# Kernel tuning notes

Hardware: AMD Instinct MI355X
Metric: run time of the kernel (lower is better)

The kernel has to match this reference:

```python
import jax, jax.numpy as jnp
import numpy as np


def setup_inputs() -> dict:
    key = jax.random.key(0)
    ks = jax.random.split(key, 7)
    B, T, D, H = 32, 512, 512, 512
    return {
        "x": jax.random.normal(ks[0], (B, T, D), dtype=jnp.float32),
        "W_Du": jax.random.normal(ks[1], (D, H), dtype=jnp.float32) * (1.0 / np.sqrt(D)),
        "W_Dr1": jax.random.normal(ks[2], (D, H), dtype=jnp.float32) * (1.0 / np.sqrt(D)),
        "W_Dr2": jax.random.normal(ks[3], (D, H), dtype=jnp.float32) * (1.0 / np.sqrt(D)),
        "b_Du": jax.random.normal(ks[4], (H,), dtype=jnp.float32) * 0.02,
        "b_Dr1": jax.random.normal(ks[5], (H,), dtype=jnp.float32) * 0.02,
        "b_Dr2": jax.random.normal(ks[6], (H,), dtype=jnp.float32) * 0.02,
    }


def reference(x, W_Du, W_Dr1, W_Dr2, b_Du, b_Dr1, b_Dr2):
    # Precompute all per-step projections across time (batched matmuls),
    # then run the strictly sequential gated recurrence with lax.scan.
    r1 = jax.nn.softmax(jnp.einsum('btd,dh->bth', x, W_Dr1) + b_Dr1, axis=-1)  # [B,T,H]
    r2 = jax.nn.softmax(jnp.einsum('btd,dh->bth', x, W_Dr2) + b_Dr2, axis=-1)  # [B,T,H]
    u = jnp.tanh(jnp.einsum('btd,dh->bth', x, W_Du) + b_Du)                     # [B,T,H]

    def step(s, inp):
        r1t, r2t, ut = inp
        s_new = r1t * s + r2t * ut
        return s_new, s_new

    init = jnp.zeros((x.shape[0], W_Du.shape[1]), dtype=x.dtype)
    # time-major for scan: [T,B,H]
    _, ys = jax.lax.scan(
        step, init,
        (jnp.swapaxes(r1, 0, 1), jnp.swapaxes(r2, 0, 1), jnp.swapaxes(u, 0, 1)),
    )
    return jnp.swapaxes(ys, 0, 1)  # [B,T,H]
```

## Files before the change

kernel.cpp:

```cpp
#include <hip/hip_runtime.h>
#include <hip/hip_bf16.h>

#define B_N 32
#define T_N 512
#define D_N 512
#define H_N 512
#define M_N (B_N * T_N)

typedef __attribute__((ext_vector_type(8))) short bf16x8;
typedef __attribute__((ext_vector_type(4))) float f32x4;

__device__ __forceinline__ unsigned short f2bf(float f) {
  unsigned u = __float_as_uint(f);
  u += 0x7FFFu + ((u >> 16) & 1u);
  return (unsigned short)(u >> 16);
}
__device__ __forceinline__ float bf2f(unsigned short h) {
  return __uint_as_float(((unsigned)h) << 16);
}
__device__ __forceinline__ unsigned short f2h(float f) {
  _Float16 h = (_Float16)f;
  return *(unsigned short*)&h;
}
__device__ __forceinline__ float h2f(unsigned short u) {
  _Float16 h = *(_Float16*)&u;
  return (float)h;
}

#define GLOAD16(g, l) __builtin_amdgcn_global_load_lds( \
    (const __attribute__((address_space(1))) void*)(g), \
    (__attribute__((address_space(3))) void*)(l), 16, 0, 0)

__global__ void prep_kernel(const float* __restrict__ x,
                            const float* __restrict__ W0,
                            const float* __restrict__ W1,
                            const float* __restrict__ W2,
                            unsigned short* __restrict__ xb,
                            unsigned short* __restrict__ Wt) {
  int blk = blockIdx.x;
  int tid = threadIdx.x;
  if (blk < 768) {
    __shared__ float tile[32][33];
    int id = blk >> 8;
    int t = blk & 255;
    int kr = (t >> 4) << 5;
    int nc = (t & 15) << 5;
    const float* W = (id == 0) ? W0 : (id == 1) ? W1 : W2;
    unsigned short* Wo = Wt + (size_t)id * (D_N * H_N);
    int tx = tid & 31, ty0 = tid >> 5;
    for (int ty = ty0; ty < 32; ty += 8)
      tile[ty][tx] = W[(size_t)(kr + ty) * H_N + nc + tx];
    __syncthreads();
    for (int ty = ty0; ty < 32; ty += 8)
      Wo[(size_t)(nc + ty) * D_N + kr + tx] = f2bf(tile[tx][ty]);
  } else {
    int b = blk - 768;
    const float4* xv = (const float4*)x;
#pragma unroll
    for (int u = 0; u < 4; ++u) {
      int i = b * 1024 + u * 256 + tid;
      float4 v = xv[i];
      ushort4 o;
      o.x = f2bf(v.x); o.y = f2bf(v.y); o.z = f2bf(v.z); o.w = f2bf(v.w);
      ((ushort4*)xb)[i] = o;
    }
  }
}

__global__ __launch_bounds__(256) void gemm3(
    const unsigned short* __restrict__ xb,
    const unsigned short* __restrict__ Wt,
    const float* __restrict__ bDu,
    const float* __restrict__ bDr1,
    const float* __restrict__ bDr2,
    unsigned short* __restrict__ uP,
    unsigned short* __restrict__ e1P,
    unsigned short* __restrict__ e2P) {
  __shared__ __align__(16) unsigned short lA[128 * 64];
  __shared__ __align__(16) unsigned short lB[128 * 64];

  const int tid = threadIdx.x;
  const int lane = tid & 63;
  const int wv = tid >> 6;
  const int wr = wv >> 1;
  const int wc = wv & 1;
  const int g = lane >> 4;
  const int c16 = lane & 15;

  const int m0 = blockIdx.x * 128;
  const int n0 = blockIdx.y * 128;
  const int id = blockIdx.z;
  const unsigned short* Wp = Wt + (size_t)id * (D_N * H_N);

  f32x4 acc[4][4];
#pragma unroll
  for (int mt = 0; mt < 4; ++mt)
#pragma unroll
    for (int nt = 0; nt < 4; ++nt)
      acc[mt][nt] = (f32x4){0.f, 0.f, 0.f, 0.f};

  const int rowoff = tid >> 3;
  const int lsl = ((tid & 7) ^ ((tid >> 3) & 7)) * 8;
  const unsigned short* aSrc = xb + (size_t)(m0 + rowoff) * D_N + lsl;
  const unsigned short* bSrc = Wp + (size_t)(n0 + rowoff) * D_N + lsl;
  char* const lAc = (char*)lA + wv * 1024;
  char* const lBc = (char*)lB + wv * 1024;

  const int h3 = c16 & 7;

#pragma unroll 1
  for (int t = 0; t < 8; ++t) {
    const int k0 = t * 64;
#pragma unroll
    for (int i = 0; i < 4; ++i)
      GLOAD16(aSrc + (size_t)i * (32 * D_N) + k0, lAc + i * 4096);
#pragma unroll
    for (int i = 0; i < 4; ++i)
      GLOAD16(bSrc + (size_t)i * (32 * D_N) + k0, lBc + i * 4096);
    asm volatile("s_waitcnt vmcnt(0)" ::: "memory");
    __syncthreads();
#pragma unroll
    for (int kh = 0; kh < 2; ++kh) {
      const int soff = ((kh * 4 + g) ^ h3) << 4;
      bf16x8 af[4], bb[4];
#pragma unroll
      for (int mt = 0; mt < 4; ++mt)
        af[mt] = *(const bf16x8*)((const char*)lA +
                                  (wr * 64 + mt * 16 + c16) * 128 + soff);
#pragma unroll
      for (int nt = 0; nt < 4; ++nt)
        bb[nt] = *(const bf16x8*)((const char*)lB +
                                  (wc * 64 + nt * 16 + c16) * 128 + soff);
#pragma unroll
      for (int mt = 0; mt < 4; ++mt)
#pragma unroll
        for (int nt = 0; nt < 4; ++nt)
          acc[mt][nt] = __builtin_amdgcn_mfma_f32_16x16x32_bf16(
              af[mt], bb[nt], acc[mt][nt], 0, 0, 0);
    }
    __syncthreads();
  }

  const float* bp = (id == 0) ? bDu : (id == 1) ? bDr1 : bDr2;
  unsigned short* outp = (id == 0) ? uP : (id == 1) ? e1P : e2P;
  float bias[4];
#pragma unroll
  for (int nt = 0; nt < 4; ++nt)
    bias[nt] = bp[n0 + wc * 64 + nt * 16 + c16];

#pragma unroll
  for (int mt = 0; mt < 4; ++mt)
#pragma unroll
    for (int i = 0; i < 4; ++i) {
      int row = m0 + wr * 64 + mt * 16 + g * 4 + i;
      unsigned short* op = outp + (size_t)row * H_N + n0 + wc * 64 + c16;
      if (id == 0) {
#pragma unroll
        for (int nt = 0; nt < 4; ++nt)
          op[nt * 16] = f2h(tanhf(acc[mt][nt][i] + bias[nt]));
      } else {
#pragma unroll
        for (int nt = 0; nt < 4; ++nt)
          op[nt * 16] = f2h(__expf(acc[mt][nt][i] + bias[nt]));
      }
    }
}

__global__ void rowsum(const unsigned short* __restrict__ e1P,
                       const unsigned short* __restrict__ e2P,
                       float* __restrict__ iS1,
                       float* __restrict__ iS2) {
  int row = blockIdx.x * 4 + (threadIdx.x >> 6);
  int lane = threadIdx.x & 63;
  const bf16x8 v1 = *(const bf16x8*)(e1P + (size_t)row * H_N + lane * 8);
  const bf16x8 v2 = *(const bf16x8*)(e2P + (size_t)row * H_N + lane * 8);
  float s1 = 0.f, s2 = 0.f;
#pragma unroll
  for (int i = 0; i < 8; ++i) {
    s1 += h2f((unsigned short)v1[i]);
    s2 += h2f((unsigned short)v2[i]);
  }
#pragma unroll
  for (int d = 1; d < 64; d <<= 1) {
    s1 += __shfl_xor(s1, d);
    s2 += __shfl_xor(s2, d);
  }
  if (lane == 0) {
    iS1[row] = 1.f / s1;
    iS2[row] = 1.f / s2;
  }
}

__global__ void scan_pass1(const unsigned short* __restrict__ e1P,
                           const unsigned short* __restrict__ e2P,
                           const unsigned short* __restrict__ uP,
                           const float* __restrict__ iS1,
                           const float* __restrict__ iS2,
                           float* __restrict__ cP,
                           float* __restrict__ cS) {
  int gt = blockIdx.x * 256 + threadIdx.x;
  int chunk = gt >> 14;
  int r = gt & 16383;
  int b = r >> 9, h = r & 511;
  int row0 = b * T_N + chunk * 64;
  size_t idx = (size_t)row0 * H_N + h;
  float p = 1.f, s = 0.f;
#pragma unroll 4
  for (int j = 0; j < 64; ++j) {
    float a = iS1[row0 + j] * h2f(e1P[idx]);
    float cu = iS2[row0 + j] * h2f(e2P[idx]) * h2f(uP[idx]);
    s = fmaf(a, s, cu);
    p *= a;
    idx += H_N;
  }
  cP[gt] = p;
  cS[gt] = s;
}

__global__ void scan_pass3(const unsigned short* __restrict__ e1P,
                           const unsigned short* __restrict__ e2P,
                           const unsigned short* __restrict__ uP,
                           const float* __restrict__ iS1,
                           const float* __restrict__ iS2,
                           const float* __restrict__ cP,
                           const float* __restrict__ cS,
                           float* __restrict__ out) {
  int gt = blockIdx.x * 256 + threadIdx.x;
  int chunk = gt >> 14;
  int r = gt & 16383;
  int b = r >> 9, h = r & 511;
  float s = 0.f;
  for (int c2 = 0; c2 < chunk; ++c2)
    s = fmaf(cP[c2 * 16384 + r], s, cS[c2 * 16384 + r]);
  int row0 = b * T_N + chunk * 64;
  size_t idx = (size_t)row0 * H_N + h;
#pragma unroll 4
  for (int j = 0; j < 64; ++j) {
    float a = iS1[row0 + j] * h2f(e1P[idx]);
    float cu = iS2[row0 + j] * h2f(e2P[idx]) * h2f(uP[idx]);
    s = fmaf(a, s, cu);
    out[idx] = s;
    idx += H_N;
  }
}

extern "C" void kernel_launch(void* const* d_in, const int* in_sizes, int n_in,
                              void* d_out, int out_size, void* d_ws, size_t ws_size,
                              hipStream_t stream) {
  const float* x  = (const float*)d_in[0];
  const float* W0 = (const float*)d_in[1];
  const float* W1 = (const float*)d_in[2];
  const float* W2 = (const float*)d_in[3];
  const float* b0 = (const float*)d_in[4];
  const float* b1 = (const float*)d_in[5];
  const float* b2 = (const float*)d_in[6];
  float* out = (float*)d_out;

  char* ws = (char*)d_ws;
  unsigned short* xb  = (unsigned short*)ws;
  unsigned short* Wt  = (unsigned short*)(ws + 16777216);
  unsigned short* uP  = (unsigned short*)(ws + 18350080);
  unsigned short* e1P = (unsigned short*)(ws + 35127296);
  unsigned short* e2P = (unsigned short*)(ws + 51904512);
  float*          iS1 = (float*)(ws + 68681728);
  float*          iS2 = (float*)(ws + 68747264);
  float*          cP  = (float*)(ws + 68812800);
  float*          cS  = (float*)(ws + 69337088);

  prep_kernel<<<2816, 256, 0, stream>>>(x, W0, W1, W2, xb, Wt);
  gemm3<<<dim3(128, 4, 3), 256, 0, stream>>>(xb, Wt, b0, b1, b2, uP, e1P, e2P);
  rowsum<<<4096, 256, 0, stream>>>(e1P, e2P, iS1, iS2);
  scan_pass1<<<512, 256, 0, stream>>>(e1P, e2P, uP, iS1, iS2, cP, cS);
  scan_pass3<<<512, 256, 0, stream>>>(e1P, e2P, uP, iS1, iS2, cP, cS, out);
}
```

Measured before the change: 85.03 us.

## Double-buffer LDS tiles in projection GEMM and use fast exp-based tanh

Replaces the single LDS buffer in the fused three-way projection GEMM with two buffers, so global-to-LDS loads of the next K tile are issued before computing the current one, with partial vmcnt waits. This aims to hide global load latency behind MFMA work. It also swaps tanhf for an exp/reciprocal formulation in the epilogue to cut transcendental cost. LDS use grows to 64KB per block, which may lower occupancy, and the fast tanh loses some accuracy for large inputs.

```diff
diff --git a/kernel.cpp b/kernel.cpp
--- a/kernel.cpp
+++ b/kernel.cpp
@@ -76,8 +76,7 @@
     unsigned short* __restrict__ uP,
     unsigned short* __restrict__ e1P,
     unsigned short* __restrict__ e2P) {
-  __shared__ __align__(16) unsigned short lA[128 * 64];
-  __shared__ __align__(16) unsigned short lB[128 * 64];
+  __shared__ __align__(16) char smem[65536];
 
   const int tid = threadIdx.x;
   const int lane = tid & 63;
@@ -103,43 +102,68 @@
   const int lsl = ((tid & 7) ^ ((tid >> 3) & 7)) * 8;
   const unsigned short* aSrc = xb + (size_t)(m0 + rowoff) * D_N + lsl;
   const unsigned short* bSrc = Wp + (size_t)(n0 + rowoff) * D_N + lsl;
-  char* const lAc = (char*)lA + wv * 1024;
-  char* const lBc = (char*)lB + wv * 1024;
+  const int dstOff = wv * 1024;
 
   const int h3 = c16 & 7;
 
+#define STAGE(buf, kstep) do {                                           \
+    const int k0_ = (kstep) * 64;                                        \
+    _Pragma("unroll")                                                    \
+    for (int i = 0; i < 4; ++i)                                          \
+      GLOAD16(aSrc + (size_t)i * (32 * D_N) + k0_,                       \
+              smem + (buf) * 16384 + dstOff + i * 4096);                 \
+    _Pragma("unroll")                                                    \
+    for (int i = 0; i < 4; ++i)                                          \
+      GLOAD16(bSrc + (size_t)i * (32 * D_N) + k0_,                       \
+              smem + 32768 + (buf) * 16384 + dstOff + i * 4096);         \
+  } while (0)
+
+#define COMPUTE(buf) do {                                                \
+    _Pragma("unroll")                                                    \
+    for (int kh = 0; kh < 2; ++kh) {                                     \
+      const int soff = ((kh * 4 + g) ^ h3) << 4;                         \
+      bf16x8 af[4], bb[4];                                               \
+      _Pragma("unroll")                                                  \
+      for (int mt = 0; mt < 4; ++mt)                                     \
+        af[mt] = *(const bf16x8*)(smem + (buf) * 16384 +                 \
+                                  (wr * 64 + mt * 16 + c16) * 128 + soff); \
+      _Pragma("unroll")                                                  \
+      for (int nt = 0; nt < 4; ++nt)                                     \
+        bb[nt] = *(const bf16x8*)(smem + 32768 + (buf) * 16384 +         \
+                                  (wc * 64 + nt * 16 + c16) * 128 + soff); \
+      _Pragma("unroll")                                                  \
+      for (int mt = 0; mt < 4; ++mt)                                     \
+        _Pragma("unroll")                                                \
+        for (int nt = 0; nt < 4; ++nt)                                   \
+          acc[mt][nt] = __builtin_amdgcn_mfma_f32_16x16x32_bf16(         \
+              af[mt], bb[nt], acc[mt][nt], 0, 0, 0);                     \
+    }                                                                    \
+  } while (0)
+
+#define WAIT8 asm volatile("s_waitcnt vmcnt(8)" ::: "memory")
+
+  STAGE(0, 0);
 #pragma unroll 1
-  for (int t = 0; t < 8; ++t) {
-    const int k0 = t * 64;
-#pragma unroll
-    for (int i = 0; i < 4; ++i)
-      GLOAD16(aSrc + (size_t)i * (32 * D_N) + k0, lAc + i * 4096);
-#pragma unroll
-    for (int i = 0; i < 4; ++i)
-      GLOAD16(bSrc + (size_t)i * (32 * D_N) + k0, lBc + i * 4096);
-    asm volatile("s_waitcnt vmcnt(0)" ::: "memory");
-    __syncthreads();
-#pragma unroll
-    for (int kh = 0; kh < 2; ++kh) {
-      const int soff = ((kh * 4 + g) ^ h3) << 4;
-      bf16x8 af[4], bb[4];
-#pragma unroll
-      for (int mt = 0; mt < 4; ++mt)
-        af[mt] = *(const bf16x8*)((const char*)lA +
-                                  (wr * 64 + mt * 16 + c16) * 128 + soff);
-#pragma unroll
-      for (int nt = 0; nt < 4; ++nt)
-        bb[nt] = *(const bf16x8*)((const char*)lB +
-                                  (wc * 64 + nt * 16 + c16) * 128 + soff);
-#pragma unroll
-      for (int mt = 0; mt < 4; ++mt)
-#pragma unroll
-        for (int nt = 0; nt < 4; ++nt)
-          acc[mt][nt] = __builtin_amdgcn_mfma_f32_16x16x32_bf16(
-              af[mt], bb[nt], acc[mt][nt], 0, 0, 0);
-    }
-    __syncthreads();
-  }
+  for (int i = 0; i < 3; ++i) {
+    STAGE(1, 2 * i + 1);
+    WAIT8;
+    __syncthreads();
+    COMPUTE(0);
+    __syncthreads();
+    STAGE(0, 2 * i + 2);
+    WAIT8;
+    __syncthreads();
+    COMPUTE(1);
+    __syncthreads();
+  }
+  STAGE(1, 7);
+  WAIT8;
+  __syncthreads();
+  COMPUTE(0);
+  __syncthreads();
+  asm volatile("s_waitcnt vmcnt(0)" ::: "memory");
+  __syncthreads();
+  COMPUTE(1);
 
   const float* bp = (id == 0) ? bDu : (id == 1) ? bDr1 : bDr2;
   unsigned short* outp = (id == 0) ? uP : (id == 1) ? e1P : e2P;
@@ -156,14 +180,20 @@
       unsigned short* op = outp + (size_t)row * H_N + n0 + wc * 64 + c16;
       if (id == 0) {
 #pragma unroll
-        for (int nt = 0; nt < 4; ++nt)
-          op[nt * 16] = f2h(tanhf(acc[mt][nt][i] + bias[nt]));
+        for (int nt = 0; nt < 4; ++nt) {
+          float z = acc[mt][nt][i] + bias[nt];
+          float e = __expf(2.f * z);
+          op[nt * 16] = f2h(1.f - 2.f * __builtin_amdgcn_rcpf(e + 1.f));
+        }
       } else {
 #pragma unroll
         for (int nt = 0; nt < 4; ++nt)
           op[nt * 16] = f2h(__expf(acc[mt][nt][i] + bias[nt]));
       }
     }
+#undef STAGE
+#undef COMPUTE
+#undef WAIT8
 }
 
 __global__ void rowsum(const unsigned short* __restrict__ e1P,
```

Result: faster. 83.11 us (-2.3%).
